# Optimization experiments

Hardware: AMD Instinct MI355X
Metric: run time of the kernel (lower is better)

Reference implementation:

```python
import jax, jax.numpy as jnp
import numpy as np

N, D, FF, T = 131072, 128, 512, 4
EPS = 1e-5


def layernorm(x, g, b):
    m = jnp.mean(x, axis=-1, keepdims=True)
    v = jnp.mean((x - m) ** 2, axis=-1, keepdims=True)
    return (x - m) * jax.lax.rsqrt(v + EPS) * g + b


def setup_inputs() -> dict:
    key = jax.random.key(0)
    ks = jax.random.split(key, 12)
    s = 1.0 / np.sqrt(D)
    return {
        "x": jax.random.normal(ks[0], (N, D), dtype=jnp.float32),
        # attention projections (single head; nhead=1 is forced by the source's shape constraints)
        "Kw": jax.random.normal(ks[1], (D, D), dtype=jnp.float32) * s,
        "Qw": jax.random.normal(ks[2], (D, D), dtype=jnp.float32) * s,
        "Vw": jax.random.normal(ks[3], (D, D), dtype=jnp.float32) * s,
        "ln1_g": jnp.ones((D,), jnp.float32),
        "ln1_b": jnp.zeros((D,), jnp.float32),
        "ln2_g": jnp.ones((D,), jnp.float32),
        "ln2_b": jnp.zeros((D,), jnp.float32),
        "w1": jax.random.normal(ks[4], (D, FF), dtype=jnp.float32) * s,
        "b1": jnp.zeros((FF,), jnp.float32),
        "w2": jax.random.normal(ks[5], (FF, D), dtype=jnp.float32) / np.sqrt(FF),
        "b2": jnp.zeros((D,), jnp.float32),
        "out_w": jax.random.normal(ks[6], (D, D), dtype=jnp.float32) * s,
        "out_b": jnp.zeros((D,), jnp.float32),
    }


def reference(x, Kw, Qw, Vw, ln1_g, ln1_b, ln2_g, ln2_b, w1, b1, w2, b2, out_w, out_b):
    for _ in range(T):  # same params reused every timestep, as in the source
        # --- softmax-free attention sublayer ---
        h = layernorm(x, ln1_g, ln1_b)
        Q = h @ Qw
        K = h @ Kw
        V = h @ Vw
        # (Q @ K^T) @ V == Q @ (K^T @ V): no softmax, so reassociate to O(n*d^2)
        x = x + Q @ (K.T @ V)
        # --- feed-forward sublayer (Linear-ReLU-Linear implied by dim_ff) ---
        h = layernorm(x, ln2_g, ln2_b)
        x = x + (jax.nn.relu(h @ w1 + b1) @ w2 + b2)
    return x @ out_w + out_b
```

## Files before the change

kernel.cpp:

```cpp
#include <hip/hip_runtime.h>

#define NROWS 131072
#define DIM   128
#define FFD   512
#define TSTEPS 4
#define NBLK  512
#define CHUNK 128
#define NCHUNK 2
#define NSLOT 16
#define SH    136

static_assert((long)NBLK * CHUNK * NCHUNK == NROWS, "grid/chunk mismatch");

typedef short          s8v   __attribute__((ext_vector_type(8)));
typedef float          f4v   __attribute__((ext_vector_type(4)));
typedef unsigned short u16x4 __attribute__((ext_vector_type(4)));

#define MFMA16(a,b,c) __builtin_amdgcn_mfma_f32_16x16x32_bf16((a),(b),(c),0,0,0)

__device__ __forceinline__ unsigned short f2bf(float f){
    unsigned u = __builtin_bit_cast(unsigned, f);
    u += 0x7FFFu + ((u >> 16) & 1u);
    return (unsigned short)(u >> 16);
}
__device__ __forceinline__ float bf2f(unsigned short h){
    return __builtin_bit_cast(float, (unsigned)h << 16);
}
__device__ __forceinline__ f4v ntload4(const float* p){
    return __builtin_nontemporal_load((const f4v*)p);
}
__device__ __forceinline__ void ntstore4(float* p, f4v v){
    __builtin_nontemporal_store(v, (f4v*)p);
}

__global__ __launch_bounds__(512, 2)
void kA(const float* __restrict__ x, const unsigned short* __restrict__ Kwp,
        const unsigned short* __restrict__ Vwp,
        const float* __restrict__ ga, const float* __restrict__ be,
        float* __restrict__ slots)
{
    __shared__ unsigned short hh[128*SH];
    __shared__ unsigned short hl[128*SH];
    __shared__ unsigned short KT[128*SH];
    __shared__ unsigned short VT[128*SH];
    const int tid  = threadIdx.x;
    const int wv   = tid >> 6, lane = tid & 63;
    const int quad = lane >> 4, l15 = lane & 15;
    const int lp   = lane >> 3, lr = lane & 7;
    const int myrow = wv*8 + lr;
    const int pc    = wv*16 + l15;

    s8v bfK[4], bfV[4];
    #pragma unroll
    for (int ks = 0; ks < 4; ++ks) {
        bfK[ks] = *(const s8v*)(Kwp + pc*DIM + ks*32 + quad*8);
        bfV[ks] = *(const s8v*)(Vwp + pc*DIM + ks*32 + quad*8);
    }

    f4v acc[8];
    #pragma unroll
    for (int i = 0; i < 8; ++i) acc[i] = (f4v){0.f,0.f,0.f,0.f};

    for (int ch = 0; ch < NCHUNK; ++ch) {
        const size_t r0 = ((size_t)blockIdx.x*NCHUNK + ch)*CHUNK;
        #pragma unroll
        for (int pp = 0; pp < 2; ++pp) {
            const int row = pp*64 + myrow;
            float v[16];
            #pragma unroll
            for (int j = 0; j < 4; ++j) {
                const f4v t = ntload4(x + (r0 + row)*DIM + lp*16 + j*4);
                v[j*4+0] = t[0]; v[j*4+1] = t[1]; v[j*4+2] = t[2]; v[j*4+3] = t[3];
            }
            float s = 0.f, q = 0.f;
            #pragma unroll
            for (int i = 0; i < 16; ++i) { s += v[i]; q += v[i]*v[i]; }
            #pragma unroll
            for (int o = 8; o < 64; o <<= 1) { s += __shfl_xor(s, o); q += __shfl_xor(q, o); }
            const float m  = s * (1.0f/128.0f);
            const float rs = rsqrtf(q * (1.0f/128.0f) - m*m + 1e-5f);
            unsigned short hi16[16], lo16[16];
            #pragma unroll
            for (int j = 0; j < 4; ++j) {
                const float4 g = *(const float4*)(ga + lp*16 + j*4);
                const float4 b = *(const float4*)(be + lp*16 + j*4);
                float hv0 = (v[j*4+0]-m)*rs*g.x + b.x;
                float hv1 = (v[j*4+1]-m)*rs*g.y + b.y;
                float hv2 = (v[j*4+2]-m)*rs*g.z + b.z;
                float hv3 = (v[j*4+3]-m)*rs*g.w + b.w;
                hi16[j*4+0] = f2bf(hv0); lo16[j*4+0] = f2bf(hv0 - bf2f(hi16[j*4+0]));
                hi16[j*4+1] = f2bf(hv1); lo16[j*4+1] = f2bf(hv1 - bf2f(hi16[j*4+1]));
                hi16[j*4+2] = f2bf(hv2); lo16[j*4+2] = f2bf(hv2 - bf2f(hi16[j*4+2]));
                hi16[j*4+3] = f2bf(hv3); lo16[j*4+3] = f2bf(hv3 - bf2f(hi16[j*4+3]));
            }
            #pragma unroll
            for (int j = 0; j < 2; ++j) {
                *(s8v*)&hh[row*SH + lp*16 + j*8] = *(const s8v*)&hi16[j*8];
                *(s8v*)&hl[row*SH + lp*16 + j*8] = *(const s8v*)&lo16[j*8];
            }
        }
        __syncthreads();
        #pragma unroll
        for (int p = 0; p < 2; ++p) {
            const s8v* bf = p ? bfV : bfK;
            unsigned short* T = p ? VT : KT;
            #pragma unroll
            for (int mt = 0; mt < 8; ++mt) {
                s8v ah[4], al[4];
                #pragma unroll
                for (int ks = 0; ks < 4; ++ks) {
                    ah[ks] = *(const s8v*)(&hh[(mt*16 + l15)*SH + ks*32 + quad*8]);
                    al[ks] = *(const s8v*)(&hl[(mt*16 + l15)*SH + ks*32 + quad*8]);
                }
                f4v c = {0.f,0.f,0.f,0.f};
                #pragma unroll
                for (int ks = 0; ks < 4; ++ks) c = MFMA16(ah[ks], bf[ks], c);
                #pragma unroll
                for (int ks = 0; ks < 4; ++ks) c = MFMA16(al[ks], bf[ks], c);
                u16x4 w4 = { f2bf(c[0]), f2bf(c[1]), f2bf(c[2]), f2bf(c[3]) };
                *(u16x4*)&T[pc*SH + mt*16 + quad*4] = w4;
            }
        }
        __syncthreads();
        #pragma unroll
        for (int ks = 0; ks < 4; ++ks) {
            const s8v af = *(const s8v*)(&KT[pc*SH + ks*32 + quad*8]);
            #pragma unroll
            for (int jt = 0; jt < 8; ++jt) {
                const s8v bfr = *(const s8v*)(&VT[(jt*16 + l15)*SH + ks*32 + quad*8]);
                acc[jt] = MFMA16(af, bfr, acc[jt]);
            }
        }
        __syncthreads();
    }
    float* S = slots + (size_t)(blockIdx.x & (NSLOT-1)) * 16384;
    #pragma unroll
    for (int jt = 0; jt < 8; ++jt) {
        const int i0 = wv*16 + quad*4;
        const int j  = jt*16 + l15;
        #pragma unroll
        for (int rg = 0; rg < 4; ++rg)
            atomicAdd(&S[(i0 + rg)*DIM + j], acc[jt][rg]);
    }
}

__global__ void kReduce(const float* __restrict__ slots, float* __restrict__ ktv)
{
    const int e = blockIdx.x*256 + threadIdx.x;
    float s = 0.f;
    #pragma unroll
    for (int b = 0; b < NSLOT; ++b) s += slots[(size_t)b*16384 + e];
    ktv[e] = s;
}

__global__ void kBuildM(const float* __restrict__ Qw, const float* __restrict__ ktv,
                        unsigned short* __restrict__ Mp, unsigned short* __restrict__ Ml)
{
    const int idx = blockIdx.x*256 + threadIdx.x;
    const int j = idx >> 7, k = idx & 127;
    float s = 0.f;
    for (int i = 0; i < 128; ++i) s += Qw[k*128 + i] * ktv[i*128 + j];
    const unsigned short hi = f2bf(s);
    Mp[idx] = hi;
    Ml[idx] = f2bf(s - bf2f(hi));
}

__global__ __launch_bounds__(512, 2)
void kB(const float* __restrict__ xin, float* __restrict__ xout,
        const unsigned short* __restrict__ Mp, const unsigned short* __restrict__ Ml,
        const float* __restrict__ g1a, const float* __restrict__ b1a,
        const float* __restrict__ g2a, const float* __restrict__ b2a,
        const unsigned short* __restrict__ w1p, const float* __restrict__ fb1,
        const unsigned short* __restrict__ w2p, const float* __restrict__ fb2)
{
    __shared__ float          xb[128*132];
    __shared__ unsigned short hs[128*SH];
    __shared__ unsigned short fbuf[128*SH];
    unsigned short* const hl = fbuf;
    const int tid  = threadIdx.x;
    const int wv   = tid >> 6, lane = tid & 63;
    const int quad = lane >> 4, l15 = lane & 15;
    const int lp   = lane >> 3, lr = lane & 7;
    const int myrow = wv*8 + lr;
    const int cg    = wv*16 + l15;

    s8v bh[4], bl[4];
    #pragma unroll
    for (int ks = 0; ks < 4; ++ks) {
        bh[ks] = *(const s8v*)(Mp + cg*DIM + ks*32 + quad*8);
        bl[ks] = *(const s8v*)(Ml + cg*DIM + ks*32 + quad*8);
    }

    for (int ch = 0; ch < NCHUNK; ++ch) {
        const size_t r0 = ((size_t)blockIdx.x*NCHUNK + ch)*CHUNK;
        #pragma unroll
        for (int i = 0; i < 8; ++i) {
            const int idx = tid + i*512;
            const int r = idx >> 5, c = (idx & 31)*4;
            const f4v t = ntload4(xin + (r0 + r)*DIM + c);
            *(f4v*)&xb[r*132 + c] = t;
        }
        __syncthreads();
        #pragma unroll
        for (int pp = 0; pp < 2; ++pp) {
            const int row = pp*64 + myrow;
            float v[16];
            #pragma unroll
            for (int j = 0; j < 4; ++j)
                *(float4*)&v[j*4] = *(const float4*)&xb[row*132 + lp*16 + j*4];
            float s = 0.f, q = 0.f;
            #pragma unroll
            for (int i = 0; i < 16; ++i) { s += v[i]; q += v[i]*v[i]; }
            #pragma unroll
            for (int o = 8; o < 64; o <<= 1) { s += __shfl_xor(s, o); q += __shfl_xor(q, o); }
            const float m  = s * (1.0f/128.0f);
            const float rs = rsqrtf(q * (1.0f/128.0f) - m*m + 1e-5f);
            unsigned short hi16[16], lo16[16];
            #pragma unroll
            for (int j = 0; j < 4; ++j) {
                const float4 g = *(const float4*)(g1a + lp*16 + j*4);
                const float4 b = *(const float4*)(b1a + lp*16 + j*4);
                float hv0 = (v[j*4+0]-m)*rs*g.x + b.x;
                float hv1 = (v[j*4+1]-m)*rs*g.y + b.y;
                float hv2 = (v[j*4+2]-m)*rs*g.z + b.z;
                float hv3 = (v[j*4+3]-m)*rs*g.w + b.w;
                hi16[j*4+0] = f2bf(hv0); lo16[j*4+0] = f2bf(hv0 - bf2f(hi16[j*4+0]));
                hi16[j*4+1] = f2bf(hv1); lo16[j*4+1] = f2bf(hv1 - bf2f(hi16[j*4+1]));
                hi16[j*4+2] = f2bf(hv2); lo16[j*4+2] = f2bf(hv2 - bf2f(hi16[j*4+2]));
                hi16[j*4+3] = f2bf(hv3); lo16[j*4+3] = f2bf(hv3 - bf2f(hi16[j*4+3]));
            }
            #pragma unroll
            for (int j = 0; j < 2; ++j) {
                *(s8v*)&hs[row*SH + lp*16 + j*8] = *(const s8v*)&hi16[j*8];
                *(s8v*)&hl[row*SH + lp*16 + j*8] = *(const s8v*)&lo16[j*8];
            }
        }
        __syncthreads();
        #pragma unroll
        for (int mt = 0; mt < 8; ++mt) {
            s8v ah[4], al[4];
            #pragma unroll
            for (int ks = 0; ks < 4; ++ks) {
                ah[ks] = *(const s8v*)(&hs[(mt*16 + l15)*SH + ks*32 + quad*8]);
                al[ks] = *(const s8v*)(&hl[(mt*16 + l15)*SH + ks*32 + quad*8]);
            }
            f4v c = {0.f,0.f,0.f,0.f};
            #pragma unroll
            for (int ks = 0; ks < 4; ++ks) c = MFMA16(ah[ks], bh[ks], c);
            #pragma unroll
            for (int ks = 0; ks < 4; ++ks) c = MFMA16(ah[ks], bl[ks], c);
            #pragma unroll
            for (int ks = 0; ks < 4; ++ks) c = MFMA16(al[ks], bh[ks], c);
            #pragma unroll
            for (int rg = 0; rg < 4; ++rg)
                xb[(mt*16 + quad*4 + rg)*132 + cg] += c[rg];
        }
        __syncthreads();
        #pragma unroll
        for (int pp = 0; pp < 2; ++pp) {
            const int row = pp*64 + myrow;
            float v[16];
            #pragma unroll
            for (int j = 0; j < 4; ++j)
                *(float4*)&v[j*4] = *(const float4*)&xb[row*132 + lp*16 + j*4];
            float s = 0.f, q = 0.f;
            #pragma unroll
            for (int i = 0; i < 16; ++i) { s += v[i]; q += v[i]*v[i]; }
            #pragma unroll
            for (int o = 8; o < 64; o <<= 1) { s += __shfl_xor(s, o); q += __shfl_xor(q, o); }
            const float m  = s * (1.0f/128.0f);
            const float rs = rsqrtf(q * (1.0f/128.0f) - m*m + 1e-5f);
            unsigned short hi16[16];
            #pragma unroll
            for (int j = 0; j < 4; ++j) {
                const float4 g = *(const float4*)(g2a + lp*16 + j*4);
                const float4 b = *(const float4*)(b2a + lp*16 + j*4);
                hi16[j*4+0] = f2bf((v[j*4+0]-m)*rs*g.x + b.x);
                hi16[j*4+1] = f2bf((v[j*4+1]-m)*rs*g.y + b.y);
                hi16[j*4+2] = f2bf((v[j*4+2]-m)*rs*g.z + b.z);
                hi16[j*4+3] = f2bf((v[j*4+3]-m)*rs*g.w + b.w);
            }
            #pragma unroll
            for (int j = 0; j < 2; ++j)
                *(s8v*)&hs[row*SH + lp*16 + j*8] = *(const s8v*)&hi16[j*8];
        }
        __syncthreads();
        f4v dx2[8];
        #pragma unroll
        for (int i = 0; i < 8; ++i) dx2[i] = (f4v){0.f,0.f,0.f,0.f};
        #pragma unroll
        for (int qf = 0; qf < 4; ++qf) {
            const int ffc = qf*128 + cg;
            s8v wa[4];
            #pragma unroll
            for (int ks = 0; ks < 4; ++ks)
                wa[ks] = *(const s8v*)(w1p + ffc*DIM + ks*32 + quad*8);
            const float bias = fb1[ffc];
            #pragma unroll
            for (int mt = 0; mt < 8; ++mt) {
                s8v af[4];
                #pragma unroll
                for (int ks = 0; ks < 4; ++ks)
                    af[ks] = *(const s8v*)(&hs[(mt*16 + l15)*SH + ks*32 + quad*8]);
                f4v c = {0.f,0.f,0.f,0.f};
                #pragma unroll
                for (int ks = 0; ks < 4; ++ks) c = MFMA16(af[ks], wa[ks], c);
                #pragma unroll
                for (int rg = 0; rg < 4; ++rg) {
                    float vv = c[rg] + bias;
                    vv = vv > 0.f ? vv : 0.f;
                    fbuf[(mt*16 + quad*4 + rg)*SH + cg] = f2bf(vv);
                }
            }
            __syncthreads();
            s8v wb[4];
            #pragma unroll
            for (int ks = 0; ks < 4; ++ks)
                wb[ks] = *(const s8v*)(w2p + cg*FFD + qf*128 + ks*32 + quad*8);
            #pragma unroll
            for (int mt = 0; mt < 8; ++mt) {
                s8v af[4];
                #pragma unroll
                for (int ks = 0; ks < 4; ++ks)
                    af[ks] = *(const s8v*)(&fbuf[(mt*16 + l15)*SH + ks*32 + quad*8]);
                f4v c = dx2[mt];
                #pragma unroll
                for (int ks = 0; ks < 4; ++ks) c = MFMA16(af[ks], wb[ks], c);
                dx2[mt] = c;
            }
            __syncthreads();
        }
        {
            const float bias = fb2[cg];
            #pragma unroll
            for (int mt = 0; mt < 8; ++mt)
                #pragma unroll
                for (int rg = 0; rg < 4; ++rg)
                    xb[(mt*16 + quad*4 + rg)*132 + cg] += dx2[mt][rg] + bias;
        }
        __syncthreads();
        #pragma unroll
        for (int i = 0; i < 8; ++i) {
            const int idx = tid + i*512;
            const int r = idx >> 5, c = (idx & 31)*4;
            ntstore4(xout + (r0 + r)*DIM + c, *(const f4v*)&xb[r*132 + c]);
        }
        __syncthreads();
    }
}

#define CHUNKF 64
#define NCHUNKF 4
static_assert((long)NBLK * CHUNKF * NCHUNKF == NROWS, "kF grid mismatch");

__global__ __launch_bounds__(256, 2)
void kF(const float* __restrict__ x, const unsigned short* __restrict__ Owp,
        const float* __restrict__ ob, float* __restrict__ out)
{
    __shared__ unsigned short hh[64*SH];
    __shared__ unsigned short hl[64*SH];
    __shared__ float          xb[64*132];
    const int tid  = threadIdx.x;
    const int quad = (tid & 63) >> 4, l15 = tid & 15;
    const int wv_  = tid >> 6;

    s8v bf[2][4];
    #pragma unroll
    for (int nt = 0; nt < 2; ++nt)
        #pragma unroll
        for (int ks = 0; ks < 4; ++ks)
            bf[nt][ks] = *(const s8v*)(Owp + (wv_*32 + nt*16 + l15)*DIM + ks*32 + quad*8);

    for (int ch = 0; ch < NCHUNKF; ++ch) {
        const size_t r0 = ((size_t)blockIdx.x*NCHUNKF + ch)*CHUNKF;
        #pragma unroll
        for (int i = 0; i < 8; ++i) {
            const int idx = tid + i*256;
            const int r = idx >> 5, c = (idx & 31)*4;
            const f4v v = ntload4(x + (r0 + r)*DIM + c);
            const unsigned short h0 = f2bf(v[0]), h1 = f2bf(v[1]),
                                 h2 = f2bf(v[2]), h3 = f2bf(v[3]);
            u16x4 w4 = { h0, h1, h2, h3 };
            u16x4 l4 = { f2bf(v[0] - bf2f(h0)), f2bf(v[1] - bf2f(h1)),
                         f2bf(v[2] - bf2f(h2)), f2bf(v[3] - bf2f(h3)) };
            *(u16x4*)&hh[r*SH + c] = w4;
            *(u16x4*)&hl[r*SH + c] = l4;
        }
        __syncthreads();
        #pragma unroll
        for (int mt = 0; mt < 4; ++mt) {
            s8v ah[4], al[4];
            #pragma unroll
            for (int ks = 0; ks < 4; ++ks) {
                ah[ks] = *(const s8v*)(&hh[(mt*16 + l15)*SH + ks*32 + quad*8]);
                al[ks] = *(const s8v*)(&hl[(mt*16 + l15)*SH + ks*32 + quad*8]);
            }
            #pragma unroll
            for (int nt = 0; nt < 2; ++nt) {
                f4v c = {0.f,0.f,0.f,0.f};
                #pragma unroll
                for (int ks = 0; ks < 4; ++ks) c = MFMA16(ah[ks], bf[nt][ks], c);
                #pragma unroll
                for (int ks = 0; ks < 4; ++ks) c = MFMA16(al[ks], bf[nt][ks], c);
                const int cg = wv_*32 + nt*16 + l15;
                const float bias = ob[cg];
                #pragma unroll
                for (int rg = 0; rg < 4; ++rg)
                    xb[(mt*16 + quad*4 + rg)*132 + cg] = c[rg] + bias;
            }
        }
        __syncthreads();
        #pragma unroll
        for (int i = 0; i < 8; ++i) {
            const int idx = tid + i*256;
            const int r = idx >> 5, c = (idx & 31)*4;
            ntstore4(out + (r0 + r)*DIM + c, *(const f4v*)&xb[r*132 + c]);
        }
        __syncthreads();
    }
}

__global__ void kPack(const float* __restrict__ Kw, const float* __restrict__ Vw,
                      const float* __restrict__ Ow, const float* __restrict__ w1,
                      const float* __restrict__ w2,
                      unsigned short* __restrict__ Kwp, unsigned short* __restrict__ Vwp,
                      unsigned short* __restrict__ Owp, unsigned short* __restrict__ w1p,
                      unsigned short* __restrict__ w2p)
{
    const int t = blockIdx.x*256 + threadIdx.x;
    if (t < 16384) {
        const int n = t >> 7, k = t & 127;
        Kwp[t] = f2bf(Kw[k*128 + n]);
        Vwp[t] = f2bf(Vw[k*128 + n]);
        Owp[t] = f2bf(Ow[k*128 + n]);
    } else if (t < 16384 + 65536) {
        const int u = t - 16384;
        const int n = u >> 7, k = u & 127;
        w1p[u] = f2bf(w1[k*FFD + n]);
    } else {
        const int u = t - 16384 - 65536;
        const int n = u >> 9, k = u & 511;
        w2p[u] = f2bf(w2[k*DIM + n]);
    }
}

extern "C" void kernel_launch(void* const* d_in, const int* in_sizes, int n_in,
                              void* d_out, int out_size, void* d_ws, size_t ws_size,
                              hipStream_t stream)
{
    (void)in_sizes; (void)n_in; (void)out_size; (void)ws_size;
    const float* x_in = (const float*)d_in[0];
    const float* Kw   = (const float*)d_in[1];
    const float* Qw   = (const float*)d_in[2];
    const float* Vw   = (const float*)d_in[3];
    const float* ln1g = (const float*)d_in[4];
    const float* ln1b = (const float*)d_in[5];
    const float* ln2g = (const float*)d_in[6];
    const float* ln2b = (const float*)d_in[7];
    const float* w1   = (const float*)d_in[8];
    const float* b1   = (const float*)d_in[9];
    const float* w2   = (const float*)d_in[10];
    const float* b2   = (const float*)d_in[11];
    const float* Ow   = (const float*)d_in[12];
    const float* ob   = (const float*)d_in[13];

    char* p = (char*)d_ws;
    float* slots        = (float*)p;          p += (size_t)NSLOT*16384*4;
    float* ktv          = (float*)p;          p += 16384*4;
    unsigned short* Kwp = (unsigned short*)p; p += 16384*2;
    unsigned short* Vwp = (unsigned short*)p; p += 16384*2;
    unsigned short* Owp = (unsigned short*)p; p += 16384*2;
    unsigned short* w1p = (unsigned short*)p; p += 65536*2;
    unsigned short* w2p = (unsigned short*)p; p += 65536*2;
    unsigned short* Mp  = (unsigned short*)p; p += 16384*2;
    unsigned short* Ml  = (unsigned short*)p; p += 16384*2;

    float* X = (float*)d_out;

    kPack<<<576, 256, 0, stream>>>(Kw, Vw, Ow, w1, w2, Kwp, Vwp, Owp, w1p, w2p);

    const float* src = x_in;
    for (int t = 0; t < TSTEPS; ++t) {
        hipMemsetAsync(slots, 0, (size_t)NSLOT*16384*4, stream);
        kA<<<NBLK, 512, 0, stream>>>(src, Kwp, Vwp, ln1g, ln1b, slots);
        kReduce<<<64, 256, 0, stream>>>(slots, ktv);
        kBuildM<<<64, 256, 0, stream>>>(Qw, ktv, Mp, Ml);
        kB<<<NBLK, 512, 0, stream>>>(src, X, Mp, Ml, ln1g, ln1b, ln2g, ln2b,
                                     w1p, b1, w2p, b2);
        src = X;
    }
    kF<<<NBLK, 256, 0, stream>>>(X, Owp, ob, (float*)d_out);
}
```

Measured before the change: 1.195 ms.

## Fuse all timesteps into one cooperative persistent kernel with register-resident rows

Replaces the per-timestep kA/kReduce/kBuildM/kB launches and the final projection with a single cooperative kernel that keeps each block's 512 rows resident in registers across all timesteps. Grid-wide syncs stand in for kernel boundaries, and the K^T V slot reduction plus M construction run inside the kernel on a subset of blocks, which also clear the slots. This removes repeated HBM reads and writes of x and the launch overhead. In exchange it holds 128 floats per thread in registers, uses about 136KB of LDS (one block per CU), serializes the LayerNorm work across tiles, and depends on all blocks being co-resident.

```diff
diff --git a/kernel.cpp b/kernel.cpp
--- a/kernel.cpp
+++ b/kernel.cpp
@@ -1,16 +1,14 @@
 #include <hip/hip_runtime.h>
+#include <hip/hip_cooperative_groups.h>
+
+namespace cg = cooperative_groups;
 
 #define NROWS 131072
 #define DIM   128
 #define FFD   512
 #define TSTEPS 4
-#define NBLK  512
-#define CHUNK 128
-#define NCHUNK 2
 #define NSLOT 16
 #define SH    136
-
-static_assert((long)NBLK * CHUNK * NCHUNK == NROWS, "grid/chunk mismatch");
 
 typedef short          s8v   __attribute__((ext_vector_type(8)));
 typedef float          f4v   __attribute__((ext_vector_type(4)));
@@ -33,390 +31,323 @@
     __builtin_nontemporal_store(v, (f4v*)p);
 }
 
+template<bool DO_LN, bool DO_LO>
+__device__ __forceinline__ void row_split(const f4v* xr, int rowoff,
+                                          const float* __restrict__ ga,
+                                          const float* __restrict__ be,
+                                          unsigned short* hs_, unsigned short* hl_)
+{
+    float m = 0.f, rs = 1.f;
+    if constexpr (DO_LN) {
+        float s = 0.f, q = 0.f;
+        #pragma unroll
+        for (int j = 0; j < 32; ++j) {
+            const f4v v = xr[j];
+            s += v[0] + v[1] + v[2] + v[3];
+            q += v[0]*v[0] + v[1]*v[1] + v[2]*v[2] + v[3]*v[3];
+        }
+        m  = s * (1.0f/128.0f);
+        rs = rsqrtf(q * (1.0f/128.0f) - m*m + 1e-5f);
+    }
+    #pragma unroll
+    for (int g2 = 0; g2 < 8; ++g2) {
+        unsigned short hi16[16], lo16[16];
+        #pragma unroll
+        for (int jj = 0; jj < 4; ++jj) {
+            const f4v v = xr[g2*4 + jj];
+            f4v gg, bb;
+            if constexpr (DO_LN) {
+                gg = *(const f4v*)(ga + g2*16 + jj*4);
+                bb = *(const f4v*)(be + g2*16 + jj*4);
+            }
+            #pragma unroll
+            for (int e = 0; e < 4; ++e) {
+                float hv;
+                if constexpr (DO_LN) hv = (v[e] - m)*rs*gg[e] + bb[e];
+                else                 hv = v[e];
+                const unsigned short h = f2bf(hv);
+                hi16[jj*4 + e] = h;
+                if constexpr (DO_LO) lo16[jj*4 + e] = f2bf(hv - bf2f(h));
+            }
+        }
+        *(s8v*)&hs_[rowoff + g2*16]     = *(const s8v*)&hi16[0];
+        *(s8v*)&hs_[rowoff + g2*16 + 8] = *(const s8v*)&hi16[8];
+        if constexpr (DO_LO) {
+            *(s8v*)&hl_[rowoff + g2*16]     = *(const s8v*)&lo16[0];
+            *(s8v*)&hl_[rowoff + g2*16 + 8] = *(const s8v*)&lo16[8];
+        }
+    }
+}
+
 __global__ __launch_bounds__(512, 2)
-void kA(const float* __restrict__ x, const unsigned short* __restrict__ Kwp,
-        const unsigned short* __restrict__ Vwp,
-        const float* __restrict__ ga, const float* __restrict__ be,
-        float* __restrict__ slots)
+void kMega(const float* __restrict__ x_in,
+           const unsigned short* __restrict__ Kwp, const unsigned short* __restrict__ Vwp,
+           const float* __restrict__ Qw,
+           const float* __restrict__ g1a, const float* __restrict__ b1a,
+           const float* __restrict__ g2a, const float* __restrict__ b2a,
+           const unsigned short* __restrict__ w1p, const float* __restrict__ fb1,
+           const unsigned short* __restrict__ w2p, const float* __restrict__ fb2,
+           const unsigned short* __restrict__ Owp, const float* __restrict__ ob,
+           float* __restrict__ slots, unsigned short* __restrict__ Mp,
+           unsigned short* __restrict__ Ml, float* __restrict__ out)
 {
-    __shared__ unsigned short hh[128*SH];
-    __shared__ unsigned short hl[128*SH];
-    __shared__ unsigned short KT[128*SH];
-    __shared__ unsigned short VT[128*SH];
+    __shared__ __align__(16) char lraw[139264];
+    unsigned short* const hs   = (unsigned short*)lraw;
+    unsigned short* const hl   = (unsigned short*)(lraw + 34816);
+    unsigned short* const fbuf = hl;
+    unsigned short* const KT   = (unsigned short*)(lraw + 69632);
+    unsigned short* const VT   = (unsigned short*)(lraw + 104448);
+    float*          const xb   = (float*)(lraw + 69632);
+    float*          const colbuf = (float*)(lraw + 69632);
+
     const int tid  = threadIdx.x;
     const int wv   = tid >> 6, lane = tid & 63;
     const int quad = lane >> 4, l15 = lane & 15;
-    const int lp   = lane >> 3, lr = lane & 7;
-    const int myrow = wv*8 + lr;
-    const int pc    = wv*16 + l15;
-
-    s8v bfK[4], bfV[4];
-    #pragma unroll
-    for (int ks = 0; ks < 4; ++ks) {
-        bfK[ks] = *(const s8v*)(Kwp + pc*DIM + ks*32 + quad*8);
-        bfV[ks] = *(const s8v*)(Vwp + pc*DIM + ks*32 + quad*8);
-    }
-
-    f4v acc[8];
-    #pragma unroll
-    for (int i = 0; i < 8; ++i) acc[i] = (f4v){0.f,0.f,0.f,0.f};
-
-    for (int ch = 0; ch < NCHUNK; ++ch) {
-        const size_t r0 = ((size_t)blockIdx.x*NCHUNK + ch)*CHUNK;
-        #pragma unroll
-        for (int pp = 0; pp < 2; ++pp) {
-            const int row = pp*64 + myrow;
-            float v[16];
-            #pragma unroll
-            for (int j = 0; j < 4; ++j) {
-                const f4v t = ntload4(x + (r0 + row)*DIM + lp*16 + j*4);
-                v[j*4+0] = t[0]; v[j*4+1] = t[1]; v[j*4+2] = t[2]; v[j*4+3] = t[3];
-            }
-            float s = 0.f, q = 0.f;
-            #pragma unroll
-            for (int i = 0; i < 16; ++i) { s += v[i]; q += v[i]*v[i]; }
-            #pragma unroll
-            for (int o = 8; o < 64; o <<= 1) { s += __shfl_xor(s, o); q += __shfl_xor(q, o); }
-            const float m  = s * (1.0f/128.0f);
-            const float rs = rsqrtf(q * (1.0f/128.0f) - m*m + 1e-5f);
-            unsigned short hi16[16], lo16[16];
-            #pragma unroll
-            for (int j = 0; j < 4; ++j) {
-                const float4 g = *(const float4*)(ga + lp*16 + j*4);
-                const float4 b = *(const float4*)(be + lp*16 + j*4);
-                float hv0 = (v[j*4+0]-m)*rs*g.x + b.x;
-                float hv1 = (v[j*4+1]-m)*rs*g.y + b.y;
-                float hv2 = (v[j*4+2]-m)*rs*g.z + b.z;
-                float hv3 = (v[j*4+3]-m)*rs*g.w + b.w;
-                hi16[j*4+0] = f2bf(hv0); lo16[j*4+0] = f2bf(hv0 - bf2f(hi16[j*4+0]));
-                hi16[j*4+1] = f2bf(hv1); lo16[j*4+1] = f2bf(hv1 - bf2f(hi16[j*4+1]));
-                hi16[j*4+2] = f2bf(hv2); lo16[j*4+2] = f2bf(hv2 - bf2f(hi16[j*4+2]));
-                hi16[j*4+3] = f2bf(hv3); lo16[j*4+3] = f2bf(hv3 - bf2f(hi16[j*4+3]));
-            }
-            #pragma unroll
-            for (int j = 0; j < 2; ++j) {
-                *(s8v*)&hh[row*SH + lp*16 + j*8] = *(const s8v*)&hi16[j*8];
-                *(s8v*)&hl[row*SH + lp*16 + j*8] = *(const s8v*)&lo16[j*8];
-            }
-        }
-        __syncthreads();
-        #pragma unroll
-        for (int p = 0; p < 2; ++p) {
-            const s8v* bf = p ? bfV : bfK;
-            unsigned short* T = p ? VT : KT;
-            #pragma unroll
-            for (int mt = 0; mt < 8; ++mt) {
-                s8v ah[4], al[4];
-                #pragma unroll
-                for (int ks = 0; ks < 4; ++ks) {
-                    ah[ks] = *(const s8v*)(&hh[(mt*16 + l15)*SH + ks*32 + quad*8]);
-                    al[ks] = *(const s8v*)(&hl[(mt*16 + l15)*SH + ks*32 + quad*8]);
-                }
-                f4v c = {0.f,0.f,0.f,0.f};
-                #pragma unroll
-                for (int ks = 0; ks < 4; ++ks) c = MFMA16(ah[ks], bf[ks], c);
-                #pragma unroll
-                for (int ks = 0; ks < 4; ++ks) c = MFMA16(al[ks], bf[ks], c);
-                u16x4 w4 = { f2bf(c[0]), f2bf(c[1]), f2bf(c[2]), f2bf(c[3]) };
-                *(u16x4*)&T[pc*SH + mt*16 + quad*4] = w4;
-            }
-        }
-        __syncthreads();
-        #pragma unroll
-        for (int ks = 0; ks < 4; ++ks) {
-            const s8v af = *(const s8v*)(&KT[pc*SH + ks*32 + quad*8]);
-            #pragma unroll
-            for (int jt = 0; jt < 8; ++jt) {
-                const s8v bfr = *(const s8v*)(&VT[(jt*16 + l15)*SH + ks*32 + quad*8]);
-                acc[jt] = MFMA16(af, bfr, acc[jt]);
-            }
-        }
-        __syncthreads();
-    }
-    float* S = slots + (size_t)(blockIdx.x & (NSLOT-1)) * 16384;
-    #pragma unroll
-    for (int jt = 0; jt < 8; ++jt) {
-        const int i0 = wv*16 + quad*4;
-        const int j  = jt*16 + l15;
-        #pragma unroll
-        for (int rg = 0; rg < 4; ++rg)
-            atomicAdd(&S[(i0 + rg)*DIM + j], acc[jt][rg]);
-    }
-}
-
-__global__ void kReduce(const float* __restrict__ slots, float* __restrict__ ktv)
-{
-    const int e = blockIdx.x*256 + threadIdx.x;
-    float s = 0.f;
-    #pragma unroll
-    for (int b = 0; b < NSLOT; ++b) s += slots[(size_t)b*16384 + e];
-    ktv[e] = s;
-}
-
-__global__ void kBuildM(const float* __restrict__ Qw, const float* __restrict__ ktv,
-                        unsigned short* __restrict__ Mp, unsigned short* __restrict__ Ml)
-{
-    const int idx = blockIdx.x*256 + threadIdx.x;
-    const int j = idx >> 7, k = idx & 127;
-    float s = 0.f;
-    for (int i = 0; i < 128; ++i) s += Qw[k*128 + i] * ktv[i*128 + j];
-    const unsigned short hi = f2bf(s);
-    Mp[idx] = hi;
-    Ml[idx] = f2bf(s - bf2f(hi));
-}
-
-__global__ __launch_bounds__(512, 2)
-void kB(const float* __restrict__ xin, float* __restrict__ xout,
-        const unsigned short* __restrict__ Mp, const unsigned short* __restrict__ Ml,
-        const float* __restrict__ g1a, const float* __restrict__ b1a,
-        const float* __restrict__ g2a, const float* __restrict__ b2a,
-        const unsigned short* __restrict__ w1p, const float* __restrict__ fb1,
-        const unsigned short* __restrict__ w2p, const float* __restrict__ fb2)
-{
-    __shared__ float          xb[128*132];
-    __shared__ unsigned short hs[128*SH];
-    __shared__ unsigned short fbuf[128*SH];
-    unsigned short* const hl = fbuf;
-    const int tid  = threadIdx.x;
-    const int wv   = tid >> 6, lane = tid & 63;
-    const int quad = lane >> 4, l15 = lane & 15;
-    const int lp   = lane >> 3, lr = lane & 7;
-    const int myrow = wv*8 + lr;
-    const int cg    = wv*16 + l15;
-
-    s8v bh[4], bl[4];
-    #pragma unroll
-    for (int ks = 0; ks < 4; ++ks) {
-        bh[ks] = *(const s8v*)(Mp + cg*DIM + ks*32 + quad*8);
-        bl[ks] = *(const s8v*)(Ml + cg*DIM + ks*32 + quad*8);
-    }
-
-    for (int ch = 0; ch < NCHUNK; ++ch) {
-        const size_t r0 = ((size_t)blockIdx.x*NCHUNK + ch)*CHUNK;
+    const int myTile = tid >> 7, myRow = tid & 127;
+    const int cgc  = wv*16 + l15;
+    const int b    = blockIdx.x;
+    const int rowoff = myRow * SH;
+
+    cg::grid_group grid = cg::this_grid();
+
+    f4v xr[32];
+    for (int p = 0; p < 4; ++p) {
+        const size_t r0 = (size_t)b*512 + (size_t)p*128;
         #pragma unroll
         for (int i = 0; i < 8; ++i) {
             const int idx = tid + i*512;
             const int r = idx >> 5, c = (idx & 31)*4;
-            const f4v t = ntload4(xin + (r0 + r)*DIM + c);
-            *(f4v*)&xb[r*132 + c] = t;
+            *(f4v*)&xb[r*132 + c] = ntload4(x_in + (r0 + r)*DIM + c);
         }
         __syncthreads();
-        #pragma unroll
-        for (int pp = 0; pp < 2; ++pp) {
-            const int row = pp*64 + myrow;
-            float v[16];
-            #pragma unroll
-            for (int j = 0; j < 4; ++j)
-                *(float4*)&v[j*4] = *(const float4*)&xb[row*132 + lp*16 + j*4];
-            float s = 0.f, q = 0.f;
-            #pragma unroll
-            for (int i = 0; i < 16; ++i) { s += v[i]; q += v[i]*v[i]; }
-            #pragma unroll
-            for (int o = 8; o < 64; o <<= 1) { s += __shfl_xor(s, o); q += __shfl_xor(q, o); }
-            const float m  = s * (1.0f/128.0f);
-            const float rs = rsqrtf(q * (1.0f/128.0f) - m*m + 1e-5f);
-            unsigned short hi16[16], lo16[16];
-            #pragma unroll
-            for (int j = 0; j < 4; ++j) {
-                const float4 g = *(const float4*)(g1a + lp*16 + j*4);
-                const float4 b = *(const float4*)(b1a + lp*16 + j*4);
-                float hv0 = (v[j*4+0]-m)*rs*g.x + b.x;
-                float hv1 = (v[j*4+1]-m)*rs*g.y + b.y;
-                float hv2 = (v[j*4+2]-m)*rs*g.z + b.z;
-                float hv3 = (v[j*4+3]-m)*rs*g.w + b.w;
-                hi16[j*4+0] = f2bf(hv0); lo16[j*4+0] = f2bf(hv0 - bf2f(hi16[j*4+0]));
-                hi16[j*4+1] = f2bf(hv1); lo16[j*4+1] = f2bf(hv1 - bf2f(hi16[j*4+1]));
-                hi16[j*4+2] = f2bf(hv2); lo16[j*4+2] = f2bf(hv2 - bf2f(hi16[j*4+2]));
-                hi16[j*4+3] = f2bf(hv3); lo16[j*4+3] = f2bf(hv3 - bf2f(hi16[j*4+3]));
-            }
-            #pragma unroll
-            for (int j = 0; j < 2; ++j) {
-                *(s8v*)&hs[row*SH + lp*16 + j*8] = *(const s8v*)&hi16[j*8];
-                *(s8v*)&hl[row*SH + lp*16 + j*8] = *(const s8v*)&lo16[j*8];
-            }
+        if (myTile == p) {
+            #pragma unroll
+            for (int j = 0; j < 32; ++j) xr[j] = *(const f4v*)&xb[myRow*132 + j*4];
         }
         __syncthreads();
-        #pragma unroll
-        for (int mt = 0; mt < 8; ++mt) {
-            s8v ah[4], al[4];
+    }
+
+    s8v bfK[4], bfV[4];
+    #pragma unroll
+    for (int ks = 0; ks < 4; ++ks) {
+        bfK[ks] = *(const s8v*)(Kwp + cgc*DIM + ks*32 + quad*8);
+        bfV[ks] = *(const s8v*)(Vwp + cgc*DIM + ks*32 + quad*8);
+    }
+
+    for (int ts = 0; ts < TSTEPS; ++ts) {
+        {
+            f4v acc[8];
+            #pragma unroll
+            for (int i = 0; i < 8; ++i) acc[i] = (f4v){0.f,0.f,0.f,0.f};
+            for (int p = 0; p < 4; ++p) {
+                if (myTile == p)
+                    row_split<true, true>(xr, rowoff, g1a, b1a, hs, hl);
+                __syncthreads();
+                #pragma unroll
+                for (int pv = 0; pv < 2; ++pv) {
+                    const s8v* bf = pv ? bfV : bfK;
+                    unsigned short* T = pv ? VT : KT;
+                    #pragma unroll
+                    for (int mt = 0; mt < 8; ++mt) {
+                        s8v ah[4], al[4];
+                        #pragma unroll
+                        for (int ks = 0; ks < 4; ++ks) {
+                            ah[ks] = *(const s8v*)(&hs[(mt*16 + l15)*SH + ks*32 + quad*8]);
+                            al[ks] = *(const s8v*)(&hl[(mt*16 + l15)*SH + ks*32 + quad*8]);
+                        }
+                        f4v c = {0.f,0.f,0.f,0.f};
+                        #pragma unroll
+                        for (int ks = 0; ks < 4; ++ks) c = MFMA16(ah[ks], bf[ks], c);
+                        #pragma unroll
+                        for (int ks = 0; ks < 4; ++ks) c = MFMA16(al[ks], bf[ks], c);
+                        u16x4 w4 = { f2bf(c[0]), f2bf(c[1]), f2bf(c[2]), f2bf(c[3]) };
+                        *(u16x4*)&T[cgc*SH + mt*16 + quad*4] = w4;
+                    }
+                }
+                __syncthreads();
+                #pragma unroll
+                for (int ks = 0; ks < 4; ++ks) {
+                    const s8v af = *(const s8v*)(&KT[cgc*SH + ks*32 + quad*8]);
+                    #pragma unroll
+                    for (int jt = 0; jt < 8; ++jt) {
+                        const s8v bfr = *(const s8v*)(&VT[(jt*16 + l15)*SH + ks*32 + quad*8]);
+                        acc[jt] = MFMA16(af, bfr, acc[jt]);
+                    }
+                }
+                __syncthreads();
+            }
+            float* S = slots + (size_t)(b & (NSLOT-1)) * 16384;
+            #pragma unroll
+            for (int jt = 0; jt < 8; ++jt) {
+                const int i0 = wv*16 + quad*4;
+                const int j  = jt*16 + l15;
+                #pragma unroll
+                for (int rg = 0; rg < 4; ++rg)
+                    atomicAdd(&S[(i0 + rg)*DIM + j], acc[jt][rg]);
+            }
+        }
+        __threadfence();
+        grid.sync();
+        if (b < 32) {
+            const int jj = tid >> 7;
+            const int ii = tid & 127;
+            const int j  = b*4 + jj;
+            float s = 0.f;
+            for (int sl = 0; sl < NSLOT; ++sl) {
+                float* ptr = slots + (size_t)sl*16384 + ii*128 + j;
+                s += *ptr;
+                *ptr = 0.f;
+            }
+            colbuf[jj*128 + ii] = s;
+            __syncthreads();
+            const int k = ii;
+            float a2 = 0.f;
+            for (int i = 0; i < 128; ++i) a2 += Qw[k*128 + i] * colbuf[jj*128 + i];
+            const unsigned short hi = f2bf(a2);
+            Mp[j*128 + k] = hi;
+            Ml[j*128 + k] = f2bf(a2 - bf2f(hi));
+            __syncthreads();
+        }
+        __threadfence();
+        grid.sync();
+        {
+            s8v bh[4], bl[4];
             #pragma unroll
             for (int ks = 0; ks < 4; ++ks) {
-                ah[ks] = *(const s8v*)(&hs[(mt*16 + l15)*SH + ks*32 + quad*8]);
-                al[ks] = *(const s8v*)(&hl[(mt*16 + l15)*SH + ks*32 + quad*8]);
-            }
-            f4v c = {0.f,0.f,0.f,0.f};
-            #pragma unroll
-            for (int ks = 0; ks < 4; ++ks) c = MFMA16(ah[ks], bh[ks], c);
-            #pragma unroll
-            for (int ks = 0; ks < 4; ++ks) c = MFMA16(ah[ks], bl[ks], c);
-            #pragma unroll
-            for (int ks = 0; ks < 4; ++ks) c = MFMA16(al[ks], bh[ks], c);
-            #pragma unroll
-            for (int rg = 0; rg < 4; ++rg)
-                xb[(mt*16 + quad*4 + rg)*132 + cg] += c[rg];
-        }
-        __syncthreads();
-        #pragma unroll
-        for (int pp = 0; pp < 2; ++pp) {
-            const int row = pp*64 + myrow;
-            float v[16];
-            #pragma unroll
-            for (int j = 0; j < 4; ++j)
-                *(float4*)&v[j*4] = *(const float4*)&xb[row*132 + lp*16 + j*4];
-            float s = 0.f, q = 0.f;
-            #pragma unroll
-            for (int i = 0; i < 16; ++i) { s += v[i]; q += v[i]*v[i]; }
-            #pragma unroll
-            for (int o = 8; o < 64; o <<= 1) { s += __shfl_xor(s, o); q += __shfl_xor(q, o); }
-            const float m  = s * (1.0f/128.0f);
-            const float rs = rsqrtf(q * (1.0f/128.0f) - m*m + 1e-5f);
-            unsigned short hi16[16];
-            #pragma unroll
-            for (int j = 0; j < 4; ++j) {
-                const float4 g = *(const float4*)(g2a + lp*16 + j*4);
-                const float4 b = *(const float4*)(b2a + lp*16 + j*4);
-                hi16[j*4+0] = f2bf((v[j*4+0]-m)*rs*g.x + b.x);
-                hi16[j*4+1] = f2bf((v[j*4+1]-m)*rs*g.y + b.y);
-                hi16[j*4+2] = f2bf((v[j*4+2]-m)*rs*g.z + b.z);
-                hi16[j*4+3] = f2bf((v[j*4+3]-m)*rs*g.w + b.w);
-            }
-            #pragma unroll
-            for (int j = 0; j < 2; ++j)
-                *(s8v*)&hs[row*SH + lp*16 + j*8] = *(const s8v*)&hi16[j*8];
-        }
-        __syncthreads();
-        f4v dx2[8];
-        #pragma unroll
-        for (int i = 0; i < 8; ++i) dx2[i] = (f4v){0.f,0.f,0.f,0.f};
-        #pragma unroll
-        for (int qf = 0; qf < 4; ++qf) {
-            const int ffc = qf*128 + cg;
-            s8v wa[4];
-            #pragma unroll
-            for (int ks = 0; ks < 4; ++ks)
-                wa[ks] = *(const s8v*)(w1p + ffc*DIM + ks*32 + quad*8);
-            const float bias = fb1[ffc];
-            #pragma unroll
-            for (int mt = 0; mt < 8; ++mt) {
-                s8v af[4];
-                #pragma unroll
-                for (int ks = 0; ks < 4; ++ks)
-                    af[ks] = *(const s8v*)(&hs[(mt*16 + l15)*SH + ks*32 + quad*8]);
-                f4v c = {0.f,0.f,0.f,0.f};
-                #pragma unroll
-                for (int ks = 0; ks < 4; ++ks) c = MFMA16(af[ks], wa[ks], c);
-                #pragma unroll
-                for (int rg = 0; rg < 4; ++rg) {
-                    float vv = c[rg] + bias;
-                    vv = vv > 0.f ? vv : 0.f;
-                    fbuf[(mt*16 + quad*4 + rg)*SH + cg] = f2bf(vv);
-                }
-            }
-            __syncthreads();
-            s8v wb[4];
-            #pragma unroll
-            for (int ks = 0; ks < 4; ++ks)
-                wb[ks] = *(const s8v*)(w2p + cg*FFD + qf*128 + ks*32 + quad*8);
-            #pragma unroll
-            for (int mt = 0; mt < 8; ++mt) {
-                s8v af[4];
-                #pragma unroll
-                for (int ks = 0; ks < 4; ++ks)
-                    af[ks] = *(const s8v*)(&fbuf[(mt*16 + l15)*SH + ks*32 + quad*8]);
-                f4v c = dx2[mt];
-                #pragma unroll
-                for (int ks = 0; ks < 4; ++ks) c = MFMA16(af[ks], wb[ks], c);
-                dx2[mt] = c;
-            }
-            __syncthreads();
-        }
-        {
-            const float bias = fb2[cg];
-            #pragma unroll
-            for (int mt = 0; mt < 8; ++mt)
-                #pragma unroll
-                for (int rg = 0; rg < 4; ++rg)
-                    xb[(mt*16 + quad*4 + rg)*132 + cg] += dx2[mt][rg] + bias;
-        }
-        __syncthreads();
-        #pragma unroll
-        for (int i = 0; i < 8; ++i) {
-            const int idx = tid + i*512;
-            const int r = idx >> 5, c = (idx & 31)*4;
-            ntstore4(xout + (r0 + r)*DIM + c, *(const f4v*)&xb[r*132 + c]);
-        }
-        __syncthreads();
-    }
-}
-
-#define CHUNKF 64
-#define NCHUNKF 4
-static_assert((long)NBLK * CHUNKF * NCHUNKF == NROWS, "kF grid mismatch");
-
-__global__ __launch_bounds__(256, 2)
-void kF(const float* __restrict__ x, const unsigned short* __restrict__ Owp,
-        const float* __restrict__ ob, float* __restrict__ out)
-{
-    __shared__ unsigned short hh[64*SH];
-    __shared__ unsigned short hl[64*SH];
-    __shared__ float          xb[64*132];
-    const int tid  = threadIdx.x;
-    const int quad = (tid & 63) >> 4, l15 = tid & 15;
-    const int wv_  = tid >> 6;
-
-    s8v bf[2][4];
-    #pragma unroll
-    for (int nt = 0; nt < 2; ++nt)
+                bh[ks] = *(const s8v*)(Mp + cgc*DIM + ks*32 + quad*8);
+                bl[ks] = *(const s8v*)(Ml + cgc*DIM + ks*32 + quad*8);
+            }
+            for (int p = 0; p < 4; ++p) {
+                if (myTile == p) {
+                    #pragma unroll
+                    for (int j = 0; j < 32; ++j) *(f4v*)&xb[myRow*132 + j*4] = xr[j];
+                    row_split<true, true>(xr, rowoff, g1a, b1a, hs, hl);
+                }
+                __syncthreads();
+                #pragma unroll
+                for (int mt = 0; mt < 8; ++mt) {
+                    s8v ah[4], al[4];
+                    #pragma unroll
+                    for (int ks = 0; ks < 4; ++ks) {
+                        ah[ks] = *(const s8v*)(&hs[(mt*16 + l15)*SH + ks*32 + quad*8]);
+                        al[ks] = *(const s8v*)(&hl[(mt*16 + l15)*SH + ks*32 + quad*8]);
+                    }
+                    f4v c = {0.f,0.f,0.f,0.f};
+                    #pragma unroll
+                    for (int ks = 0; ks < 4; ++ks) c = MFMA16(ah[ks], bh[ks], c);
+                    #pragma unroll
+                    for (int ks = 0; ks < 4; ++ks) c = MFMA16(ah[ks], bl[ks], c);
+                    #pragma unroll
+                    for (int ks = 0; ks < 4; ++ks) c = MFMA16(al[ks], bh[ks], c);
+                    #pragma unroll
+                    for (int rg = 0; rg < 4; ++rg)
+                        xb[(mt*16 + quad*4 + rg)*132 + cgc] += c[rg];
+                }
+                __syncthreads();
+                if (myTile == p) {
+                    #pragma unroll
+                    for (int j = 0; j < 32; ++j) xr[j] = *(const f4v*)&xb[myRow*132 + j*4];
+                    row_split<true, false>(xr, rowoff, g2a, b2a, hs, nullptr);
+                }
+                __syncthreads();
+                f4v dx2[8];
+                #pragma unroll
+                for (int i = 0; i < 8; ++i) dx2[i] = (f4v){0.f,0.f,0.f,0.f};
+                #pragma unroll
+                for (int qf = 0; qf < 4; ++qf) {
+                    s8v wa[4];
+                    #pragma unroll
+                    for (int ks = 0; ks < 4; ++ks)
+                        wa[ks] = *(const s8v*)(w1p + (qf*128 + cgc)*DIM + ks*32 + quad*8);
+                    const float bias = fb1[qf*128 + cgc];
+                    #pragma unroll
+                    for (int mt = 0; mt < 8; ++mt) {
+                        s8v af[4];
+                        #pragma unroll
+                        for (int ks = 0; ks < 4; ++ks)
+                            af[ks] = *(const s8v*)(&hs[(mt*16 + l15)*SH + ks*32 + quad*8]);
+                        f4v c = {0.f,0.f,0.f,0.f};
+                        #pragma unroll
+                        for (int ks = 0; ks < 4; ++ks) c = MFMA16(af[ks], wa[ks], c);
+                        #pragma unroll
+                        for (int rg = 0; rg < 4; ++rg) {
+                            float vv = c[rg] + bias;
+                            vv = vv > 0.f ? vv : 0.f;
+                            fbuf[(mt*16 + quad*4 + rg)*SH + cgc] = f2bf(vv);
+                        }
+                    }
+                    __syncthreads();
+                    s8v wb[4];
+                    #pragma unroll
+                    for (int ks = 0; ks < 4; ++ks)
+                        wb[ks] = *(const s8v*)(w2p + cgc*FFD + qf*128 + ks*32 + quad*8);
+                    #pragma unroll
+                    for (int mt = 0; mt < 8; ++mt) {
+                        s8v af[4];
+                        #pragma unroll
+                        for (int ks = 0; ks < 4; ++ks)
+                            af[ks] = *(const s8v*)(&fbuf[(mt*16 + l15)*SH + ks*32 + quad*8]);
+                        f4v c = dx2[mt];
+                        #pragma unroll
+                        for (int ks = 0; ks < 4; ++ks) c = MFMA16(af[ks], wb[ks], c);
+                        dx2[mt] = c;
+                    }
+                    __syncthreads();
+                }
+                {
+                    const float bias = fb2[cgc];
+                    #pragma unroll
+                    for (int mt = 0; mt < 8; ++mt)
+                        #pragma unroll
+                        for (int rg = 0; rg < 4; ++rg)
+                            xb[(mt*16 + quad*4 + rg)*132 + cgc] += dx2[mt][rg] + bias;
+                }
+                __syncthreads();
+                if (myTile == p) {
+                    #pragma unroll
+                    for (int j = 0; j < 32; ++j) xr[j] = *(const f4v*)&xb[myRow*132 + j*4];
+                }
+                __syncthreads();
+            }
+        }
+    }
+    {
+        s8v bfO[4];
         #pragma unroll
         for (int ks = 0; ks < 4; ++ks)
-            bf[nt][ks] = *(const s8v*)(Owp + (wv_*32 + nt*16 + l15)*DIM + ks*32 + quad*8);
-
-    for (int ch = 0; ch < NCHUNKF; ++ch) {
-        const size_t r0 = ((size_t)blockIdx.x*NCHUNKF + ch)*CHUNKF;
-        #pragma unroll
-        for (int i = 0; i < 8; ++i) {
-            const int idx = tid + i*256;
-            const int r = idx >> 5, c = (idx & 31)*4;
-            const f4v v = ntload4(x + (r0 + r)*DIM + c);
-            const unsigned short h0 = f2bf(v[0]), h1 = f2bf(v[1]),
-                                 h2 = f2bf(v[2]), h3 = f2bf(v[3]);
-            u16x4 w4 = { h0, h1, h2, h3 };
-            u16x4 l4 = { f2bf(v[0] - bf2f(h0)), f2bf(v[1] - bf2f(h1)),
-                         f2bf(v[2] - bf2f(h2)), f2bf(v[3] - bf2f(h3)) };
-            *(u16x4*)&hh[r*SH + c] = w4;
-            *(u16x4*)&hl[r*SH + c] = l4;
-        }
-        __syncthreads();
-        #pragma unroll
-        for (int mt = 0; mt < 4; ++mt) {
-            s8v ah[4], al[4];
-            #pragma unroll
-            for (int ks = 0; ks < 4; ++ks) {
-                ah[ks] = *(const s8v*)(&hh[(mt*16 + l15)*SH + ks*32 + quad*8]);
-                al[ks] = *(const s8v*)(&hl[(mt*16 + l15)*SH + ks*32 + quad*8]);
-            }
-            #pragma unroll
-            for (int nt = 0; nt < 2; ++nt) {
+            bfO[ks] = *(const s8v*)(Owp + cgc*DIM + ks*32 + quad*8);
+        const float biasO = ob[cgc];
+        for (int p = 0; p < 4; ++p) {
+            if (myTile == p)
+                row_split<false, true>(xr, rowoff, nullptr, nullptr, hs, hl);
+            __syncthreads();
+            #pragma unroll
+            for (int mt = 0; mt < 8; ++mt) {
+                s8v ah[4], al[4];
+                #pragma unroll
+                for (int ks = 0; ks < 4; ++ks) {
+                    ah[ks] = *(const s8v*)(&hs[(mt*16 + l15)*SH + ks*32 + quad*8]);
+                    al[ks] = *(const s8v*)(&hl[(mt*16 + l15)*SH + ks*32 + quad*8]);
+                }
                 f4v c = {0.f,0.f,0.f,0.f};
                 #pragma unroll
-                for (int ks = 0; ks < 4; ++ks) c = MFMA16(ah[ks], bf[nt][ks], c);
-                #pragma unroll
-                for (int ks = 0; ks < 4; ++ks) c = MFMA16(al[ks], bf[nt][ks], c);
-                const int cg = wv_*32 + nt*16 + l15;
-                const float bias = ob[cg];
+                for (int ks = 0; ks < 4; ++ks) c = MFMA16(ah[ks], bfO[ks], c);
+                #pragma unroll
+                for (int ks = 0; ks < 4; ++ks) c = MFMA16(al[ks], bfO[ks], c);
                 #pragma unroll
                 for (int rg = 0; rg < 4; ++rg)
-                    xb[(mt*16 + quad*4 + rg)*132 + cg] = c[rg] + bias;
-            }
-        }
-        __syncthreads();
-        #pragma unroll
-        for (int i = 0; i < 8; ++i) {
-            const int idx = tid + i*256;
-            const int r = idx >> 5, c = (idx & 31)*4;
-            ntstore4(out + (r0 + r)*DIM + c, *(const f4v*)&xb[r*132 + c]);
-        }
-        __syncthreads();
+                    xb[(mt*16 + quad*4 + rg)*132 + cgc] = c[rg] + biasO;
+            }
+            __syncthreads();
+            const size_t r0 = (size_t)b*512 + (size_t)p*128;
+            #pragma unroll
+            for (int i = 0; i < 8; ++i) {
+                const int idx = tid + i*512;
+                const int r = idx >> 5, c = (idx & 31)*4;
+                ntstore4(out + (r0 + r)*DIM + c, *(const f4v*)&xb[r*132 + c]);
+            }
+            __syncthreads();
+        }
     }
 }
 
@@ -466,7 +397,6 @@
 
     char* p = (char*)d_ws;
     float* slots        = (float*)p;          p += (size_t)NSLOT*16384*4;
-    float* ktv          = (float*)p;          p += 16384*4;
     unsigned short* Kwp = (unsigned short*)p; p += 16384*2;
     unsigned short* Vwp = (unsigned short*)p; p += 16384*2;
     unsigned short* Owp = (unsigned short*)p; p += 16384*2;
@@ -475,19 +405,18 @@
     unsigned short* Mp  = (unsigned short*)p; p += 16384*2;
     unsigned short* Ml  = (unsigned short*)p; p += 16384*2;
 
-    float* X = (float*)d_out;
+    float* out = (float*)d_out;
 
     kPack<<<576, 256, 0, stream>>>(Kw, Vw, Ow, w1, w2, Kwp, Vwp, Owp, w1p, w2p);
-
-    const float* src = x_in;
-    for (int t = 0; t < TSTEPS; ++t) {
-        hipMemsetAsync(slots, 0, (size_t)NSLOT*16384*4, stream);
-        kA<<<NBLK, 512, 0, stream>>>(src, Kwp, Vwp, ln1g, ln1b, slots);
-        kReduce<<<64, 256, 0, stream>>>(slots, ktv);
-        kBuildM<<<64, 256, 0, stream>>>(Qw, ktv, Mp, Ml);
-        kB<<<NBLK, 512, 0, stream>>>(src, X, Mp, Ml, ln1g, ln1b, ln2g, ln2b,
-                                     w1p, b1, w2p, b2);
-        src = X;
-    }
-    kF<<<NBLK, 256, 0, stream>>>(X, Owp, ob, (float*)d_out);
-}
+    (void)hipMemsetAsync(slots, 0, (size_t)NSLOT*16384*4, stream);
+
+    void* args[] = {
+        (void*)&x_in, (void*)&Kwp, (void*)&Vwp, (void*)&Qw,
+        (void*)&ln1g, (void*)&ln1b, (void*)&ln2g, (void*)&ln2b,
+        (void*)&w1p, (void*)&b1, (void*)&w2p, (void*)&b2,
+        (void*)&Owp, (void*)&ob, (void*)&slots, (void*)&Mp,
+        (void*)&Ml, (void*)&out
+    };
+    (void)hipLaunchCooperativeKernel((const void*)kMega, dim3(256), dim3(512),
+                                     args, 0, stream);
+}
```

Measured after the change: 1.806 ms. 51.1% more time.
